# Kernel tuning notes

Measured on AMD Instinct MI355X. Metric: run time of the kernel, lower is better.

## Reference

```python
import jax, jax.numpy as jnp
import numpy as np

B, T, D = 4, 2048, 1024
NF = 512
NB = 4
FREQ_SCALE = 0.1


def _w(k, shape, scale):
    return jax.random.normal(k, shape, jnp.float32) * scale


def setup_inputs() -> dict:
    key = jax.random.key(0)
    ks = jax.random.split(key, 16)
    d = D ** -0.5
    inp = {}
    inp['x'] = jax.random.normal(ks[0], (B, T, D), jnp.float32)
    inp['norm_g'] = jnp.ones((D,), jnp.float32)
    inp['norm_b'] = jnp.zeros((D,), jnp.float32)
    inp['Wconcept'] = _w(ks[1], (D, D), d); inp['bconcept'] = jnp.zeros((D,), jnp.float32)
    inp['Wcg'] = _w(ks[2], (D, D), d); inp['bcg'] = jnp.zeros((D,), jnp.float32)
    inp['Wfg'] = _w(ks[3], (NF, D), d); inp['bfg'] = jnp.zeros((NF,), jnp.float32)
    inp['Wtg'] = _w(ks[4], (1, D), d); inp['btg'] = jnp.zeros((1,), jnp.float32)
    inp['Wband'] = _w(ks[5], (NB, D), d); inp['bband'] = jnp.zeros((NB,), jnp.float32)
    inp['Wsp'] = _w(ks[6], (2 * NF, D), d)  # to_spectral, no bias
    inp['freq_importance'] = jnp.ones((NF,), jnp.float32)
    inp['log_decay'] = (jnp.linspace(-3.0, -0.001, NF) + _w(ks[7], (NF,), 0.1)).astype(jnp.float32)
    inp['frequencies'] = ((jnp.arange(NF, dtype=jnp.float32) / NF * 2.0 - 1.0) * 0.2)
    inp['dt'] = jnp.ones((NF,), jnp.float32) * 0.5
    inp['Wgate'] = _w(ks[8], (D, D), d); inp['bgate'] = jnp.zeros((D,), jnp.float32)
    inp['Wfs'] = _w(ks[9], (D, 2 * NF), (2 * NF) ** -0.5)  # from_spectral, no bias
    inp['output_scale'] = jnp.ones((1,), jnp.float32) * 0.5
    inp['norm2_g'] = jnp.ones((D,), jnp.float32)
    inp['norm2_b'] = jnp.zeros((D,), jnp.float32)
    inp['W1'] = _w(ks[10], (4 * D, D), d); inp['b1'] = jnp.zeros((4 * D,), jnp.float32)
    inp['W2'] = _w(ks[11], (D, 4 * D), (4 * D) ** -0.5); inp['b2'] = jnp.zeros((D,), jnp.float32)
    return inp


def _ln(x, g, b):
    m = jnp.mean(x, axis=-1, keepdims=True)
    v = jnp.var(x, axis=-1, keepdims=True)
    return (x - m) * jax.lax.rsqrt(v + 1e-5) * g + b


def reference(x, norm_g, norm_b, Wconcept, bconcept, Wcg, bcg, Wfg, bfg, Wtg, btg,
              Wband, bband, Wsp, freq_importance, log_decay, frequencies, dt,
              Wgate, bgate, Wfs, output_scale, norm2_g, norm2_b, W1, b1, W2, b2):
    b_, t_, _ = x.shape
    nf = log_decay.shape[0]
    nb = Wband.shape[0]
    residual = x
    xn = _ln(x, norm_g, norm_b)

    concept = xn @ Wconcept.T + bconcept
    concept_preserved = concept * jax.nn.sigmoid(xn @ Wcg.T + bcg)

    forget_gates = jax.nn.sigmoid(xn @ Wfg.T + bfg)          # (B,T,NF)
    temporal_strength = jax.nn.sigmoid(xn @ Wtg.T + btg)     # (B,T,1)
    band_strengths = jax.nn.sigmoid(xn @ Wband.T + bband)    # (B,T,NB)

    sp = xn @ Wsp.T                                          # (B,T,2*NF)
    u = jax.lax.complex(sp[..., :nf], sp[..., nf:]) * forget_gates

    decay = jax.nn.sigmoid(log_decay) * (jax.nn.softmax(freq_importance) * nf)
    omega = frequencies * FREQ_SCALE * (jax.nn.sigmoid(dt) * 2.0)
    rot = jax.lax.complex(jnp.cos(omega), jnp.sin(omega))    # (NF,)
    A = decay * rot                                          # (NF,) complex

    band_scale = jnp.repeat(band_strengths, nf // nb, axis=-1)  # (B,T,NF)
    A_exp = A * band_scale                                   # (B,T,NF) complex

    ones_first = jnp.ones((b_, 1, nf), A_exp.dtype)
    powers = jnp.cumprod(jnp.concatenate([ones_first, A_exp[:, :-1, :]], axis=1), axis=1)
    powers = powers * temporal_strength
    kernel = powers * rot

    n_fft = 2 * t_
    Uf = jnp.fft.fft(u, n=n_fft, axis=1)
    Kf = jnp.fft.fft(kernel, n=n_fft, axis=1)
    y = jnp.fft.ifft(Uf * Kf, n=n_fft, axis=1)[:, :t_, :]

    spectral_out = jnp.concatenate([y.real, y.imag], axis=-1)
    y_proj = (spectral_out @ Wfs.T) * output_scale
    gate_values = jax.nn.sigmoid(xn @ Wgate.T + bgate)
    y_gated = (y_proj * gate_values + concept_preserved) / 2.0  # dropout: eval mode

    x2 = residual + y_gated
    xn2 = _ln(x2, norm2_g, norm2_b)
    h = jax.nn.gelu(xn2 @ W1.T + b1, approximate=False)
    return x2 + h @ W2.T + b2
```

## Files before the change

kernel.cpp:

```cpp
#include <hip/hip_runtime.h>
#include <hip/hip_bf16.h>
#include <cstdint>
#include <cstddef>

typedef unsigned short u16;
typedef unsigned int u32;
typedef short bf16x8 __attribute__((ext_vector_type(8)));
typedef float f32x4 __attribute__((ext_vector_type(4)));
typedef float f32x2 __attribute__((ext_vector_type(2)));

static constexpr int Bb = 4, Tt = 2048, Dd = 1024, NFf = 512, NBb = 4;
static constexpr int Mm = Bb * Tt;
static constexpr int NZz = 4736;
static constexpr int Lc = 32;

#define DEV __device__ __forceinline__

typedef const __attribute__((address_space(1))) u32* gas_p;
typedef __attribute__((address_space(3))) u32* las_p;

DEV u16 f2bf(float f) {
    uint32_t u = __float_as_uint(f);
    u = (u + 0x7FFF + ((u >> 16) & 1)) >> 16;
    return (u16)u;
}
DEV float bf2f(u16 h) { return __uint_as_float(((uint32_t)h) << 16); }
DEV float sigm(float x) { return 1.0f / (1.0f + __expf(-x)); }
DEV float gelu_ex(float t) { return 0.5f * t * (1.0f + erff(t * 0.70710678118f)); }

static constexpr int NW0 = NZz * Dd;
static constexpr int NW1 = Dd * 2 * NFf;
static constexpr int NW2 = 4 * Dd * Dd;
static constexpr int NW3 = 4 * Dd * Dd;
static constexpr int NWB_CAT = NW0 / 1024;
static constexpr int NCVT = (NW1 + NW2 + NW3) / 1024;

__global__ __launch_bounds__(256) void prep_all(
    const float* __restrict__ Wconcept, const float* __restrict__ Wcg,
    const float* __restrict__ Wfg, const float* __restrict__ Wgate,
    const float* __restrict__ Wsp, const float* __restrict__ Wtg,
    const float* __restrict__ Wband,
    const float* __restrict__ bconcept, const float* __restrict__ bcg,
    const float* __restrict__ bfg, const float* __restrict__ bgate,
    const float* __restrict__ btg, const float* __restrict__ bband,
    const float* __restrict__ fi, const float* __restrict__ logd,
    const float* __restrict__ freqs, const float* __restrict__ dtv,
    const float* __restrict__ x, const float* __restrict__ norm_g,
    const float* __restrict__ norm_b,
    u16* __restrict__ wcat, float* __restrict__ bias_cat,
    float* __restrict__ rr, float* __restrict__ ri,
    float* __restrict__ Ar, float* __restrict__ Ai,
    u16* __restrict__ xn)
{
    const int bx = blockIdx.x;
    if (bx == 0) {
        __shared__ float red[256];
        int t = threadIdx.x;
        float v0 = fi[t], v1 = fi[t + 256];
        red[t] = fmaxf(v0, v1); __syncthreads();
        for (int s = 128; s; s >>= 1) { if (t < s) red[t] = fmaxf(red[t], red[t + s]); __syncthreads(); }
        float mx = red[0]; __syncthreads();
        float e0 = expf(v0 - mx), e1 = expf(v1 - mx);
        red[t] = e0 + e1; __syncthreads();
        for (int s = 128; s; s >>= 1) { if (t < s) red[t] += red[t + s]; __syncthreads(); }
        float inv = 1.0f / red[0];
#pragma unroll
        for (int k = 0; k < 2; k++) {
            int f = t + k * 256;
            float e = k ? e1 : e0;
            float decay = sigm(logd[f]) * (e * inv * (float)NFf);
            float omega = freqs[f] * 0.1f * (sigm(dtv[f]) * 2.0f);
            float cc = cosf(omega), ss = sinf(omega);
            rr[f] = cc; ri[f] = ss; Ar[f] = decay * cc; Ai[f] = decay * ss;
        }
        return;
    }
    if (bx <= NWB_CAT) {
        const int i = ((bx - 1) * 256 + threadIdx.x) * 4;
        int r = i >> 10, c = i & 1023;
        float4 v = {0.f, 0.f, 0.f, 0.f};
        if      (r < 1024) v = *(const float4*)(Wconcept + r * 1024 + c);
        else if (r < 2048) v = *(const float4*)(Wcg + (r - 1024) * 1024 + c);
        else if (r < 2560) v = *(const float4*)(Wfg + (r - 2048) * 1024 + c);
        else if (r < 3584) v = *(const float4*)(Wgate + (r - 2560) * 1024 + c);
        else if (r < 4608) v = *(const float4*)(Wsp + (r - 3584) * 1024 + c);
        else if (r == 4608) v = *(const float4*)(Wtg + c);
        else if (r < 4613) v = *(const float4*)(Wband + (r - 4609) * 1024 + c);
        *(ushort4*)(wcat + i) = ushort4{f2bf(v.x), f2bf(v.y), f2bf(v.z), f2bf(v.w)};
        if (c == 0) {
            float bv;
            if      (r < 1024) bv = bconcept[r];
            else if (r < 2048) bv = bcg[r - 1024];
            else if (r < 2560) bv = bfg[r - 2048];
            else if (r < 3584) bv = bgate[r - 2560];
            else if (r < 4608) bv = 0.0f;
            else if (r == 4608) bv = btg[0];
            else if (r < 4613) bv = bband[r - 4609];
            else bv = 0.0f;
            bias_cat[r] = bv;
        }
        return;
    }
    const int m = bx - NWB_CAT - 1, tid = threadIdx.x;
    float4 v = ((const float4*)(x + (size_t)m * Dd))[tid];
    float s1 = v.x + v.y + v.z + v.w;
    float s2 = v.x * v.x + v.y * v.y + v.z * v.z + v.w * v.w;
    __shared__ float lds[16];
    for (int o = 32; o; o >>= 1) { s1 += __shfl_down(s1, o); s2 += __shfl_down(s2, o); }
    int lane = tid & 63, w = tid >> 6;
    if (!lane) { lds[w] = s1; lds[8 + w] = s2; }
    __syncthreads();
    s1 = lds[0] + lds[1] + lds[2] + lds[3];
    s2 = lds[8] + lds[9] + lds[10] + lds[11];
    float mean = s1 * (1.0f / Dd);
    float var  = s2 * (1.0f / Dd) - mean * mean;
    float rstd = rsqrtf(var + 1e-5f);
    float4 gv = ((const float4*)norm_g)[tid];
    float4 bv = ((const float4*)norm_b)[tid];
    ushort4 o;
    o.x = f2bf((v.x - mean) * rstd * gv.x + bv.x);
    o.y = f2bf((v.y - mean) * rstd * gv.y + bv.y);
    o.z = f2bf((v.z - mean) * rstd * gv.z + bv.z);
    o.w = f2bf((v.w - mean) * rstd * gv.w + bv.w);
    ((ushort4*)(xn + (size_t)m * Dd))[tid] = o;
}

template<int MODE>
DEV void gemm_body(int m0, int n0,
                   u16* __restrict__ smA, u16* __restrict__ smB,
                   const u16* __restrict__ A, const u16* __restrict__ Bw,
                   const float* __restrict__ bias, const u16* __restrict__ addb,
                   void* __restrict__ Cout, int M, int N, int K)
{
    const int tid = threadIdx.x;
    const int w = tid >> 6, lane = tid & 63;
    const int wr = w >> 1, wc = w & 1;
    const int quad = lane >> 4, l16 = lane & 15;

    const int r0 = tid >> 3;
    const int cs = (tid & 7) ^ (r0 & 7);
    const u16* gA = A + (size_t)(m0 + r0) * K + cs * 8;
    const u16* gB = Bw + (size_t)(n0 + r0) * K + cs * 8;

    const int swzf = l16 & 7;

    f32x4 acc[4][4];
#pragma unroll
    for (int i = 0; i < 4; i++)
#pragma unroll
        for (int j = 0; j < 4; j++) acc[i][j] = {0.f, 0.f, 0.f, 0.f};

    for (int k0 = 0; k0 < K; k0 += 64) {
        __syncthreads();
#pragma unroll
        for (int j = 0; j < 4; j++) {
            __builtin_amdgcn_global_load_lds((gas_p)(gA + k0 + (size_t)(j * 32) * K),
                                             (las_p)(smA + j * 2048 + tid * 8), 16, 0, 0);
            __builtin_amdgcn_global_load_lds((gas_p)(gB + k0 + (size_t)(j * 32) * K),
                                             (las_p)(smB + j * 2048 + tid * 8), 16, 0, 0);
        }
        __syncthreads();
#pragma unroll
        for (int seg = 0; seg < 2; seg++) {
            bf16x8 af[4], bfv[4];
#pragma unroll
            for (int mi = 0; mi < 4; mi++)
                af[mi] = *(const bf16x8*)&smA[(wr * 64 + mi * 16 + l16) * 64 +
                                              (((seg * 4 + quad) ^ swzf) * 8)];
#pragma unroll
            for (int ni = 0; ni < 4; ni++)
                bfv[ni] = *(const bf16x8*)&smB[(wc * 64 + ni * 16 + l16) * 64 +
                                               (((seg * 4 + quad) ^ swzf) * 8)];
#pragma unroll
            for (int mi = 0; mi < 4; mi++)
#pragma unroll
                for (int ni = 0; ni < 4; ni++)
                    acc[mi][ni] = __builtin_amdgcn_mfma_f32_16x16x32_bf16(
                        af[mi], bfv[ni], acc[mi][ni], 0, 0, 0);
        }
    }

#pragma unroll
    for (int mi = 0; mi < 4; mi++) {
#pragma unroll
        for (int ni = 0; ni < 4; ni++) {
            const int gn = n0 + wc * 64 + ni * 16 + l16;
            const int gm0 = m0 + wr * 64 + mi * 16 + quad * 4;
            if constexpr (MODE == 0 || MODE == 2 || MODE == 4) {
                float bv = (MODE == 4) ? 0.0f : bias[gn];
                float t0 = acc[mi][ni][0] + bv, t1 = acc[mi][ni][1] + bv;
                float t2 = acc[mi][ni][2] + bv, t3 = acc[mi][ni][3] + bv;
                if constexpr (MODE == 2) {
                    t0 = gelu_ex(t0); t1 = gelu_ex(t1); t2 = gelu_ex(t2); t3 = gelu_ex(t3);
                }
                __hip_bfloat162 h01 = __float22bfloat162_rn(float2{t0, t1});
                __hip_bfloat162 h23 = __float22bfloat162_rn(float2{t2, t3});
                __hip_bfloat16* o = (__hip_bfloat16*)Cout;
                o[(size_t)(gm0 + 0) * N + gn] = h01.x;
                o[(size_t)(gm0 + 1) * N + gn] = h01.y;
                o[(size_t)(gm0 + 2) * N + gn] = h23.x;
                o[(size_t)(gm0 + 3) * N + gn] = h23.y;
            } else {
#pragma unroll
                for (int r = 0; r < 4; r++) {
                    const int gm = gm0 + r;
                    ((float*)Cout)[(size_t)gm * N + gn] =
                        acc[mi][ni][r] + bias[gn] + bf2f(addb[(size_t)gm * N + gn]);
                }
            }
        }
    }
}

template<int MODE>
__global__ __launch_bounds__(256, 3) void gemm_bt(
    const u16* __restrict__ A, const u16* __restrict__ Bw,
    const float* __restrict__ bias, const u16* __restrict__ addb,
    void* __restrict__ Cout, int M, int N, int K)
{
    __shared__ __align__(16) u16 smA[128 * 64];
    __shared__ __align__(16) u16 smB[128 * 64];
    gemm_body<MODE>(blockIdx.x * 128, blockIdx.y * 128, smA, smB,
                    A, Bw, bias, addb, Cout, M, N, K);
}

static constexpr int NG2 = (Mm / 128) * (NZz / 128);
__global__ __launch_bounds__(256, 3) void gemm_cvt0(
    const u16* __restrict__ A, const u16* __restrict__ Bw,
    const float* __restrict__ bias, void* __restrict__ Cout,
    int M, int N, int K,
    const float* __restrict__ Wfs, const float* __restrict__ W1,
    const float* __restrict__ W2,
    u16* __restrict__ wfs, u16* __restrict__ w1b, u16* __restrict__ w2b)
{
    const int bid = blockIdx.x;
    if (bid < NG2) {
        __shared__ __align__(16) u16 smA[128 * 64];
        __shared__ __align__(16) u16 smB[128 * 64];
        gemm_body<0>((bid & 63) * 128, (bid >> 6) * 128, smA, smB,
                     A, Bw, bias, nullptr, Cout, M, N, K);
        return;
    }
    const int i = (bid - NG2) * 1024 + threadIdx.x * 4;
    if (i < NW1) {
        float4 v = *(const float4*)(Wfs + i);
        *(ushort4*)(wfs + i) = ushort4{f2bf(v.x), f2bf(v.y), f2bf(v.z), f2bf(v.w)};
    } else if (i < NW1 + NW2) {
        int j = i - NW1;
        float4 v = *(const float4*)(W1 + j);
        *(ushort4*)(w1b + j) = ushort4{f2bf(v.x), f2bf(v.y), f2bf(v.z), f2bf(v.w)};
    } else {
        int j = i - NW1 - NW2;
        float4 v = *(const float4*)(W2 + j);
        *(ushort4*)(w2b + j) = ushort4{f2bf(v.x), f2bf(v.y), f2bf(v.z), f2bf(v.w)};
    }
}

__global__ __launch_bounds__(256) void conv_kernel(
    const u16* __restrict__ Z,
    const float* __restrict__ Ar, const float* __restrict__ Ai,
    const float* __restrict__ rr, const float* __restrict__ ri,
    u16* __restrict__ spec)
{
    __shared__ ushort2 su[96 * 64];
    __shared__ float stsv[Lc], sbsv[Lc];
    const int tid = threadIdx.x;
    const int fl = tid & 63;
    const int ty = tid >> 6;
    const int f0 = blockIdx.x * 64;
    const int t0 = blockIdx.y * 64;
    const int b  = blockIdx.z;
    const int band = f0 >> 7;

    if (tid < Lc) {
        stsv[tid] = sigm(bf2f(Z[(size_t)(b * Tt + tid) * NZz + 4608]));
    } else if (tid < 2 * Lc) {
        int tau = tid - Lc;
        sbsv[tau] = sigm(bf2f(Z[(size_t)(b * Tt + tau) * NZz + 4609 + band]));
    }
    for (int i = tid; i < 96 * 64; i += 256) {
        int r = i >> 6, ff = i & 63;
        int t = t0 - 32 + r;
        ushort2 v{0, 0};
        if (t >= 0) {
            const u16* zr = Z + (size_t)(b * Tt + t) * NZz;
            float fg = sigm(bf2f(zr[2048 + f0 + ff]));
            v.x = f2bf(bf2f(zr[3584 + f0 + ff]) * fg);
            v.y = f2bf(bf2f(zr[4096 + f0 + ff]) * fg);
        }
        su[i] = v;
    }
    __syncthreads();

    const float ar = Ar[f0 + fl], ai = Ai[f0 + fl];
    const float cr = rr[f0 + fl], ci = ri[f0 + fl];
    float Pr = 1.0f, Pi = 0.0f;

    const int tl0 = 32 + ty * 16;
    f32x2 win[16], y[16];
#pragma unroll
    for (int j = 0; j < 16; j++) {
        ushort2 h = su[(tl0 + j) * 64 + fl];
        win[j] = f32x2{bf2f(h.x), bf2f(h.y)};
        y[j] = f32x2{0.f, 0.f};
    }
#pragma unroll
    for (int tau = 0; tau < Lc; tau++) {
        float tsv = stsv[tau];
        float kr = tsv * (cr * Pr - ci * Pi);
        float ki = tsv * (cr * Pi + ci * Pr);
#pragma unroll
        for (int j = 0; j < 16; j++) {
            y[j].x += win[j].x * kr - win[j].y * ki;
            y[j].y += win[j].x * ki + win[j].y * kr;
        }
#pragma unroll
        for (int j = 15; j >= 1; j--) win[j] = win[j - 1];
        ushort2 h = su[(tl0 - tau - 1) * 64 + fl];
        win[0] = f32x2{bf2f(h.x), bf2f(h.y)};
        float bsv = sbsv[tau];
        float er = ar * bsv, ei = ai * bsv;
        float nPr = Pr * er - Pi * ei;
        float nPi = Pr * ei + Pi * er;
        Pr = nPr; Pi = nPi;
    }
#pragma unroll
    for (int j = 0; j < 16; j++) {
        size_t row = (size_t)(b * Tt + t0 + ty * 16 + j);
        spec[row * (2 * NFf) + f0 + fl]       = f2bf(y[j].x);
        spec[row * (2 * NFf) + NFf + f0 + fl] = f2bf(y[j].y);
    }
}

__global__ __launch_bounds__(256) void fuse2_ln_kernel(
    const float* __restrict__ x, const u16* __restrict__ Z,
    const u16* __restrict__ P2, const float* __restrict__ osc,
    const float* __restrict__ g2, const float* __restrict__ b2v,
    u16* __restrict__ x2b, u16* __restrict__ xn2)
{
    const int m = blockIdx.x, tid = threadIdx.x;
    const float os = osc[0];
    const u16* zr = Z + (size_t)m * NZz;
    float4 xv = ((const float4*)(x + (size_t)m * Dd))[tid];
    ushort4 pv = ((const ushort4*)(P2 + (size_t)m * Dd))[tid];
    ushort4 cv = *(const ushort4*)(zr + tid * 4);
    ushort4 gv = *(const ushort4*)(zr + 1024 + tid * 4);
    ushort4 av = *(const ushort4*)(zr + 2560 + tid * 4);
    float vals[4]; float s1 = 0.0f, s2 = 0.0f;
#pragma unroll
    for (int j = 0; j < 4; j++) {
        float concept = bf2f((&cv.x)[j]);
        float cg   = sigm(bf2f((&gv.x)[j]));
        float gate = sigm(bf2f((&av.x)[j]));
        float p = bf2f((&pv.x)[j]);
        float v = (&xv.x)[j] + 0.5f * (p * os * gate + concept * cg);
        vals[j] = v; s1 += v; s2 += v * v;
    }
    __shared__ float lds[16];
    for (int o = 32; o; o >>= 1) { s1 += __shfl_down(s1, o); s2 += __shfl_down(s2, o); }
    int lane = tid & 63, w = tid >> 6;
    if (!lane) { lds[w] = s1; lds[8 + w] = s2; }
    __syncthreads();
    s1 = lds[0] + lds[1] + lds[2] + lds[3];
    s2 = lds[8] + lds[9] + lds[10] + lds[11];
    float mean = s1 * (1.0f / Dd);
    float var  = s2 * (1.0f / Dd) - mean * mean;
    float rstd = rsqrtf(var + 1e-5f);
    ushort4 xo, no;
#pragma unroll
    for (int j = 0; j < 4; j++) {
        int d = tid * 4 + j;
        (&xo.x)[j] = f2bf(vals[j]);
        (&no.x)[j] = f2bf((vals[j] - mean) * rstd * g2[d] + b2v[d]);
    }
    ((ushort4*)(x2b + (size_t)m * Dd))[tid] = xo;
    ((ushort4*)(xn2 + (size_t)m * Dd))[tid] = no;
}

extern "C" void kernel_launch(void* const* d_in, const int* in_sizes, int n_in,
                              void* d_out, int out_size, void* d_ws, size_t ws_size,
                              hipStream_t stream)
{
    const float* x        = (const float*)d_in[0];
    const float* norm_g   = (const float*)d_in[1];
    const float* norm_b   = (const float*)d_in[2];
    const float* Wconcept = (const float*)d_in[3];
    const float* bconcept = (const float*)d_in[4];
    const float* Wcg      = (const float*)d_in[5];
    const float* bcg      = (const float*)d_in[6];
    const float* Wfg      = (const float*)d_in[7];
    const float* bfg      = (const float*)d_in[8];
    const float* Wtg      = (const float*)d_in[9];
    const float* btg      = (const float*)d_in[10];
    const float* Wband    = (const float*)d_in[11];
    const float* bband    = (const float*)d_in[12];
    const float* Wsp      = (const float*)d_in[13];
    const float* fi       = (const float*)d_in[14];
    const float* logd     = (const float*)d_in[15];
    const float* freqs    = (const float*)d_in[16];
    const float* dtv      = (const float*)d_in[17];
    const float* Wgate    = (const float*)d_in[18];
    const float* bgate    = (const float*)d_in[19];
    const float* Wfs      = (const float*)d_in[20];
    const float* osc      = (const float*)d_in[21];
    const float* n2g      = (const float*)d_in[22];
    const float* n2b      = (const float*)d_in[23];
    const float* W1       = (const float*)d_in[24];
    const float* b1       = (const float*)d_in[25];
    const float* W2       = (const float*)d_in[26];
    const float* b2       = (const float*)d_in[27];

    char* ws = (char*)d_ws;
    size_t off = 0;
    auto alloc = [&](size_t bytes) { size_t c = off; off += (bytes + 255) & ~(size_t)255; return c; };
    size_t o_wcat = alloc((size_t)NZz * Dd * 2);
    size_t o_bias = alloc((size_t)NZz * 4);
    size_t o_wfs  = alloc((size_t)Dd * 2 * NFf * 2);
    size_t o_w1   = alloc((size_t)4 * Dd * Dd * 2);
    size_t o_w2   = alloc((size_t)4 * Dd * Dd * 2);
    size_t o_xn   = alloc((size_t)Mm * Dd * 2);
    size_t o_Z    = alloc((size_t)Mm * NZz * 2);
    size_t o_u    = alloc((size_t)Mm * NFf * 4);
    size_t o_spec = alloc((size_t)Mm * Dd * 2);
    size_t o_P2   = alloc((size_t)Mm * Dd * 2);
    size_t o_rr   = alloc(NFf * 4);
    size_t o_ri   = alloc(NFf * 4);
    size_t o_Ar   = alloc(NFf * 4);
    size_t o_Ai   = alloc(NFf * 4);
    if (ws_size < off) return;

    u16*    wcat = (u16*)(ws + o_wcat);
    float*  bias = (float*)(ws + o_bias);
    u16*    wfs  = (u16*)(ws + o_wfs);
    u16*    w1b  = (u16*)(ws + o_w1);
    u16*    w2b  = (u16*)(ws + o_w2);
    u16*    xn   = (u16*)(ws + o_xn);
    u16*    Zb   = (u16*)(ws + o_Z);
    u16*    hb   = (u16*)(ws + o_Z);
    u16*    x2b  = (u16*)(ws + o_u);
    u16*    spec = (u16*)(ws + o_spec);
    u16*    xn2  = (u16*)(ws + o_spec);
    u16*    P2   = (u16*)(ws + o_P2);
    float*  rr   = (float*)(ws + o_rr);
    float*  ri   = (float*)(ws + o_ri);
    float*  Ar   = (float*)(ws + o_Ar);
    float*  Ai   = (float*)(ws + o_Ai);

    prep_all<<<1 + NWB_CAT + Mm, 256, 0, stream>>>(
        Wconcept, Wcg, Wfg, Wgate, Wsp, Wtg, Wband,
        bconcept, bcg, bfg, bgate, btg, bband,
        fi, logd, freqs, dtv,
        x, norm_g, norm_b,
        wcat, bias, rr, ri, Ar, Ai, xn);

    gemm_cvt0<<<NG2 + NCVT, 256, 0, stream>>>(
        xn, wcat, bias, (void*)Zb, Mm, NZz, Dd,
        Wfs, W1, W2, wfs, w1b, w2b);

    conv_kernel<<<dim3(NFf / 64, Tt / 64, Bb), 256, 0, stream>>>(
        Zb, Ar, Ai, rr, ri, spec);

    gemm_bt<4><<<dim3(Mm / 128, Dd / 128), 256, 0, stream>>>(
        spec, wfs, nullptr, nullptr, (void*)P2, Mm, Dd, 2 * NFf);

    fuse2_ln_kernel<<<Mm, 256, 0, stream>>>(x, Zb, P2, osc, n2g, n2b, x2b, xn2);

    gemm_bt<2><<<dim3(Mm / 128, (4 * Dd) / 128), 256, 0, stream>>>(
        xn2, w1b, b1, nullptr, (void*)hb, Mm, 4 * Dd, Dd);
    gemm_bt<3><<<dim3(Mm / 128, Dd / 128), 256, 0, stream>>>(
        hb, w2b, b2, x2b, d_out, Mm, Dd, 4 * Dd);
}
```

Baseline: 503.6 us.

## Fuse gating residual and LN2 partial sums into from_spectral GEMM epilogue

The from_spectral GEMM epilogue now applies the output scale, gate sigmoid, concept gating and residual add itself. It writes x2 in bf16 along with per-64-column partial sums for LayerNorm statistics, and a small ln2_finish kernel then normalizes. This removes the P2 intermediate round trip and moves the W1/W2 bf16 conversion into this later launch to rebalance work. The conv kernel's loads of Z are also vectorized to paired elements. The risk is that the epilogue's strided, uncoalesced gathers from Z and x may be slow, and LN2 now reads x2 after bf16 rounding.

```diff
diff --git a/kernel.cpp b/kernel.cpp
--- a/kernel.cpp
+++ b/kernel.cpp
@@ -33,7 +33,8 @@
 static constexpr int NW2 = 4 * Dd * Dd;
 static constexpr int NW3 = 4 * Dd * Dd;
 static constexpr int NWB_CAT = NW0 / 1024;
-static constexpr int NCVT = (NW1 + NW2 + NW3) / 1024;
+static constexpr int NCVT_WFS = NW1 / 1024;
+static constexpr int NCVT_MLP = (NW2 + NW3) / 1024;
 
 __global__ __launch_bounds__(256) void prep_all(
     const float* __restrict__ Wconcept, const float* __restrict__ Wcg,
@@ -130,7 +131,11 @@
                    u16* __restrict__ smA, u16* __restrict__ smB,
                    const u16* __restrict__ A, const u16* __restrict__ Bw,
                    const float* __restrict__ bias, const u16* __restrict__ addb,
-                   void* __restrict__ Cout, int M, int N, int K)
+                   void* __restrict__ Cout, int M, int N, int K,
+                   const float* __restrict__ xres = nullptr,
+                   const u16* __restrict__ Zf = nullptr,
+                   const float* __restrict__ oscp = nullptr,
+                   f32x2* __restrict__ psums = nullptr)
 {
     const int tid = threadIdx.x;
     const int w = tid >> 6, lane = tid & 63;
@@ -178,6 +183,52 @@
                     acc[mi][ni] = __builtin_amdgcn_mfma_f32_16x16x32_bf16(
                         af[mi], bfv[ni], acc[mi][ni], 0, 0, 0);
         }
+    }
+
+    if constexpr (MODE == 5) {
+        const float os = oscp[0];
+        float rs1[4][4], rs2[4][4];
+#pragma unroll
+        for (int mi = 0; mi < 4; mi++)
+#pragma unroll
+            for (int r = 0; r < 4; r++) { rs1[mi][r] = 0.f; rs2[mi][r] = 0.f; }
+#pragma unroll
+        for (int mi = 0; mi < 4; mi++) {
+#pragma unroll
+            for (int r = 0; r < 4; r++) {
+                const int gm = m0 + wr * 64 + mi * 16 + quad * 4 + r;
+                const u16* zr = Zf + (size_t)gm * NZz;
+                const float* xr = xres + (size_t)gm * Dd;
+                u16* o = (u16*)Cout;
+#pragma unroll
+                for (int ni = 0; ni < 4; ni++) {
+                    const int gn = n0 + wc * 64 + ni * 16 + l16;
+                    float p = acc[mi][ni][r];
+                    float concept = bf2f(zr[gn]);
+                    float cg   = sigm(bf2f(zr[1024 + gn]));
+                    float gate = sigm(bf2f(zr[2560 + gn]));
+                    float v = xr[gn] + 0.5f * (p * os * gate + concept * cg);
+                    rs1[mi][r] += v; rs2[mi][r] += v * v;
+                    o[(size_t)gm * Dd + gn] = f2bf(v);
+                }
+            }
+        }
+        const int nch = (n0 + wc * 64) >> 6;
+#pragma unroll
+        for (int mi = 0; mi < 4; mi++)
+#pragma unroll
+            for (int r = 0; r < 4; r++) {
+                float a = rs1[mi][r], b = rs2[mi][r];
+#pragma unroll
+                for (int o = 1; o < 16; o <<= 1) {
+                    a += __shfl_xor(a, o); b += __shfl_xor(b, o);
+                }
+                if (l16 == 0) {
+                    const int gm = m0 + wr * 64 + mi * 16 + quad * 4 + r;
+                    psums[(size_t)nch * Mm + gm] = f32x2{a, b};
+                }
+            }
+        return;
     }
 
 #pragma unroll
@@ -229,9 +280,7 @@
     const u16* __restrict__ A, const u16* __restrict__ Bw,
     const float* __restrict__ bias, void* __restrict__ Cout,
     int M, int N, int K,
-    const float* __restrict__ Wfs, const float* __restrict__ W1,
-    const float* __restrict__ W2,
-    u16* __restrict__ wfs, u16* __restrict__ w1b, u16* __restrict__ w2b)
+    const float* __restrict__ Wfs, u16* __restrict__ wfs)
 {
     const int bid = blockIdx.x;
     if (bid < NG2) {
@@ -242,18 +291,64 @@
         return;
     }
     const int i = (bid - NG2) * 1024 + threadIdx.x * 4;
-    if (i < NW1) {
-        float4 v = *(const float4*)(Wfs + i);
-        *(ushort4*)(wfs + i) = ushort4{f2bf(v.x), f2bf(v.y), f2bf(v.z), f2bf(v.w)};
-    } else if (i < NW1 + NW2) {
-        int j = i - NW1;
-        float4 v = *(const float4*)(W1 + j);
-        *(ushort4*)(w1b + j) = ushort4{f2bf(v.x), f2bf(v.y), f2bf(v.z), f2bf(v.w)};
+    float4 v = *(const float4*)(Wfs + i);
+    *(ushort4*)(wfs + i) = ushort4{f2bf(v.x), f2bf(v.y), f2bf(v.z), f2bf(v.w)};
+}
+
+static constexpr int NG5 = (Mm / 128) * (Dd / 128);
+__global__ __launch_bounds__(256, 3) void gemm_cvt5(
+    const u16* __restrict__ A, const u16* __restrict__ Bw,
+    void* __restrict__ Cout, int M, int N, int K,
+    const float* __restrict__ xres, const u16* __restrict__ Zf,
+    const float* __restrict__ oscp, f32x2* __restrict__ psums,
+    const float* __restrict__ W1, const float* __restrict__ W2,
+    u16* __restrict__ w1b, u16* __restrict__ w2b)
+{
+    const int bid = blockIdx.x;
+    if (bid < NG5) {
+        __shared__ __align__(16) u16 smA[128 * 64];
+        __shared__ __align__(16) u16 smB[128 * 64];
+        gemm_body<5>((bid & 63) * 128, (bid >> 6) * 128, smA, smB,
+                     A, Bw, nullptr, nullptr, Cout, M, N, K,
+                     xres, Zf, oscp, psums);
+        return;
+    }
+    const int i = (bid - NG5) * 1024 + threadIdx.x * 4;
+    if (i < NW2) {
+        float4 v = *(const float4*)(W1 + i);
+        *(ushort4*)(w1b + i) = ushort4{f2bf(v.x), f2bf(v.y), f2bf(v.z), f2bf(v.w)};
     } else {
-        int j = i - NW1 - NW2;
+        int j = i - NW2;
         float4 v = *(const float4*)(W2 + j);
         *(ushort4*)(w2b + j) = ushort4{f2bf(v.x), f2bf(v.y), f2bf(v.z), f2bf(v.w)};
     }
+}
+
+__global__ __launch_bounds__(256) void ln2_finish(
+    const f32x2* __restrict__ psums, const u16* __restrict__ x2b,
+    const float* __restrict__ g2, const float* __restrict__ b2v,
+    u16* __restrict__ xn2)
+{
+    const int m = blockIdx.x, tid = threadIdx.x;
+    __shared__ float sm[2];
+    if (tid < 64) {
+        f32x2 p = (tid < 16) ? psums[(size_t)tid * Mm + m] : f32x2{0.f, 0.f};
+        for (int o = 8; o; o >>= 1) { p.x += __shfl_down(p.x, o); p.y += __shfl_down(p.y, o); }
+        if (tid == 0) { sm[0] = p.x; sm[1] = p.y; }
+    }
+    __syncthreads();
+    float mean = sm[0] * (1.0f / Dd);
+    float var  = sm[1] * (1.0f / Dd) - mean * mean;
+    float rstd = rsqrtf(var + 1e-5f);
+    ushort4 h = ((const ushort4*)(x2b + (size_t)m * Dd))[tid];
+    float4 gv = ((const float4*)g2)[tid];
+    float4 bv = ((const float4*)b2v)[tid];
+    ushort4 o;
+    o.x = f2bf((bf2f(h.x) - mean) * rstd * gv.x + bv.x);
+    o.y = f2bf((bf2f(h.y) - mean) * rstd * gv.y + bv.y);
+    o.z = f2bf((bf2f(h.z) - mean) * rstd * gv.z + bv.z);
+    o.w = f2bf((bf2f(h.w) - mean) * rstd * gv.w + bv.w);
+    ((ushort4*)(xn2 + (size_t)m * Dd))[tid] = o;
 }
 
 __global__ __launch_bounds__(256) void conv_kernel(
@@ -278,17 +373,20 @@
         int tau = tid - Lc;
         sbsv[tau] = sigm(bf2f(Z[(size_t)(b * Tt + tau) * NZz + 4609 + band]));
     }
-    for (int i = tid; i < 96 * 64; i += 256) {
-        int r = i >> 6, ff = i & 63;
+    for (int i = tid; i < 96 * 32; i += 256) {
+        int r = i >> 5, fp = (i & 31) * 2;
         int t = t0 - 32 + r;
-        ushort2 v{0, 0};
+        ushort4 v{0, 0, 0, 0};
         if (t >= 0) {
             const u16* zr = Z + (size_t)(b * Tt + t) * NZz;
-            float fg = sigm(bf2f(zr[2048 + f0 + ff]));
-            v.x = f2bf(bf2f(zr[3584 + f0 + ff]) * fg);
-            v.y = f2bf(bf2f(zr[4096 + f0 + ff]) * fg);
-        }
-        su[i] = v;
+            ushort2 fg2 = *(const ushort2*)(zr + 2048 + f0 + fp);
+            ushort2 sr2 = *(const ushort2*)(zr + 3584 + f0 + fp);
+            ushort2 si2 = *(const ushort2*)(zr + 4096 + f0 + fp);
+            float g0 = sigm(bf2f(fg2.x)), g1 = sigm(bf2f(fg2.y));
+            v.x = f2bf(bf2f(sr2.x) * g0); v.y = f2bf(bf2f(si2.x) * g0);
+            v.z = f2bf(bf2f(sr2.y) * g1); v.w = f2bf(bf2f(si2.y) * g1);
+        }
+        *(ushort4*)&su[r * 64 + fp] = v;
     }
     __syncthreads();
 
@@ -330,51 +428,6 @@
         spec[row * (2 * NFf) + f0 + fl]       = f2bf(y[j].x);
         spec[row * (2 * NFf) + NFf + f0 + fl] = f2bf(y[j].y);
     }
-}
-
-__global__ __launch_bounds__(256) void fuse2_ln_kernel(
-    const float* __restrict__ x, const u16* __restrict__ Z,
-    const u16* __restrict__ P2, const float* __restrict__ osc,
-    const float* __restrict__ g2, const float* __restrict__ b2v,
-    u16* __restrict__ x2b, u16* __restrict__ xn2)
-{
-    const int m = blockIdx.x, tid = threadIdx.x;
-    const float os = osc[0];
-    const u16* zr = Z + (size_t)m * NZz;
-    float4 xv = ((const float4*)(x + (size_t)m * Dd))[tid];
-    ushort4 pv = ((const ushort4*)(P2 + (size_t)m * Dd))[tid];
-    ushort4 cv = *(const ushort4*)(zr + tid * 4);
-    ushort4 gv = *(const ushort4*)(zr + 1024 + tid * 4);
-    ushort4 av = *(const ushort4*)(zr + 2560 + tid * 4);
-    float vals[4]; float s1 = 0.0f, s2 = 0.0f;
-#pragma unroll
-    for (int j = 0; j < 4; j++) {
-        float concept = bf2f((&cv.x)[j]);
-        float cg   = sigm(bf2f((&gv.x)[j]));
-        float gate = sigm(bf2f((&av.x)[j]));
-        float p = bf2f((&pv.x)[j]);
-        float v = (&xv.x)[j] + 0.5f * (p * os * gate + concept * cg);
-        vals[j] = v; s1 += v; s2 += v * v;
-    }
-    __shared__ float lds[16];
-    for (int o = 32; o; o >>= 1) { s1 += __shfl_down(s1, o); s2 += __shfl_down(s2, o); }
-    int lane = tid & 63, w = tid >> 6;
-    if (!lane) { lds[w] = s1; lds[8 + w] = s2; }
-    __syncthreads();
-    s1 = lds[0] + lds[1] + lds[2] + lds[3];
-    s2 = lds[8] + lds[9] + lds[10] + lds[11];
-    float mean = s1 * (1.0f / Dd);
-    float var  = s2 * (1.0f / Dd) - mean * mean;
-    float rstd = rsqrtf(var + 1e-5f);
-    ushort4 xo, no;
-#pragma unroll
-    for (int j = 0; j < 4; j++) {
-        int d = tid * 4 + j;
-        (&xo.x)[j] = f2bf(vals[j]);
-        (&no.x)[j] = f2bf((vals[j] - mean) * rstd * g2[d] + b2v[d]);
-    }
-    ((ushort4*)(x2b + (size_t)m * Dd))[tid] = xo;
-    ((ushort4*)(xn2 + (size_t)m * Dd))[tid] = no;
 }
 
 extern "C" void kernel_launch(void* const* d_in, const int* in_sizes, int n_in,
@@ -422,7 +475,7 @@
     size_t o_Z    = alloc((size_t)Mm * NZz * 2);
     size_t o_u    = alloc((size_t)Mm * NFf * 4);
     size_t o_spec = alloc((size_t)Mm * Dd * 2);
-    size_t o_P2   = alloc((size_t)Mm * Dd * 2);
+    size_t o_ps   = alloc((size_t)16 * Mm * 8);
     size_t o_rr   = alloc(NFf * 4);
     size_t o_ri   = alloc(NFf * 4);
     size_t o_Ar   = alloc(NFf * 4);
@@ -440,7 +493,7 @@
     u16*    x2b  = (u16*)(ws + o_u);
     u16*    spec = (u16*)(ws + o_spec);
     u16*    xn2  = (u16*)(ws + o_spec);
-    u16*    P2   = (u16*)(ws + o_P2);
+    f32x2*  psums = (f32x2*)(ws + o_ps);
     float*  rr   = (float*)(ws + o_rr);
     float*  ri   = (float*)(ws + o_ri);
     float*  Ar   = (float*)(ws + o_Ar);
@@ -453,17 +506,17 @@
         x, norm_g, norm_b,
         wcat, bias, rr, ri, Ar, Ai, xn);
 
-    gemm_cvt0<<<NG2 + NCVT, 256, 0, stream>>>(
-        xn, wcat, bias, (void*)Zb, Mm, NZz, Dd,
-        Wfs, W1, W2, wfs, w1b, w2b);
+    gemm_cvt0<<<NG2 + NCVT_WFS, 256, 0, stream>>>(
+        xn, wcat, bias, (void*)Zb, Mm, NZz, Dd, Wfs, wfs);
 
     conv_kernel<<<dim3(NFf / 64, Tt / 64, Bb), 256, 0, stream>>>(
         Zb, Ar, Ai, rr, ri, spec);
 
-    gemm_bt<4><<<dim3(Mm / 128, Dd / 128), 256, 0, stream>>>(
-        spec, wfs, nullptr, nullptr, (void*)P2, Mm, Dd, 2 * NFf);
-
-    fuse2_ln_kernel<<<Mm, 256, 0, stream>>>(x, Zb, P2, osc, n2g, n2b, x2b, xn2);
+    gemm_cvt5<<<NG5 + NCVT_MLP, 256, 0, stream>>>(
+        spec, wfs, (void*)x2b, Mm, Dd, 2 * NFf,
+        x, Zb, osc, psums, W1, W2, w1b, w2b);
+
+    ln2_finish<<<Mm, 256, 0, stream>>>(psums, x2b, n2g, n2b, xn2);
 
     gemm_bt<2><<<dim3(Mm / 128, (4 * Dd) / 128), 256, 0, stream>>>(
         xn2, w1b, b1, nullptr, (void*)hb, Mm, 4 * Dd, Dd);
```

Result: slower. 538.5 us (+6.9%).
